# Optimization experiments

Measured on AMD Instinct MI355X. Metric: run time of the kernel, lower is better.

## Reference

```python
import jax, jax.numpy as jnp
import numpy as np

GROUP_SIZE = 64  # quantization group size along in_features (K)


def setup_inputs() -> dict:
    key = jax.random.key(0)
    k1, k2, k3, k4, k5 = jax.random.split(key, 5)
    M, K, N = 32, 8192, 8192
    num_groups = K // GROUP_SIZE
    x = jax.random.normal(k1, (M, K), dtype=jnp.float32)
    # packed int4 weights: two nibbles per byte along K -> [N, K//2]
    packed_weight = jax.random.randint(k2, (N, K // 2), 0, 256, dtype=jnp.int32)
    scales = jax.random.uniform(k3, (N, num_groups), dtype=jnp.float32) * 0.02 + 1e-3
    zeros = jax.random.uniform(k4, (N, num_groups), dtype=jnp.float32) * 15.0
    bias_param = jax.random.normal(k5, (N,), dtype=jnp.float32)
    return {"x": x, "packed_weight": packed_weight, "scales": scales,
            "zeros": zeros, "bias_param": bias_param}


def reference(x, packed_weight, scales, zeros, bias_param):
    # x: [M, K] float; packed_weight: [N, K//2] int (uint8 semantics)
    # scales/zeros: [N, num_groups]; bias_param: [N]
    K = x.shape[-1]
    k = jnp.arange(K)
    shift = (k % 2) * 4                     # low nibble for even k, high for odd
    # unpack int4: q[n, k] in [0, 15]
    q = (packed_weight[:, k // 2] >> shift[None, :]) & 15   # [N, K]
    gidx = k // GROUP_SIZE                                  # [K]
    # group-wise dequant: (q - zero) * scale
    w = (q.astype(jnp.float32) - zeros[:, gidx]) * scales[:, gidx]  # [N, K]
    out = jnp.einsum('mk,nk->mn', x, w) + bias_param[None, :]        # [M, N]
    return out
```

## Files before the change

### kernel.cpp

```cpp
#include <hip/hip_runtime.h>
#include <hip/hip_bf16.h>


#define KK 8192
#define NN 8192
#define KP 4096
#define NG 128
#define BN 16
#define KSW 64
#define NKS 256

typedef __attribute__((ext_vector_type(8))) short short8;
typedef __attribute__((ext_vector_type(4))) float floatx4;

__device__ __forceinline__ unsigned pack_bf16x2(float lo, float hi) {
    union { __hip_bfloat162 h; unsigned u; } c;
    c.h = __float22bfloat162_rn(make_float2(lo, hi));
    return c.u;
}

__global__ void xconv_kernel(const float* __restrict__ x, ushort* __restrict__ xb)
{
    const int tid = blockIdx.x * 256 + threadIdx.x;
    const int l   = tid & 63;
    const int ks  = (tid >> 6) & 255;
    const int mt  = tid >> 14;
    const int m   = (l & 15) + 16 * mt;
    const int kb  = ks * 32 + (l >> 4) * 8;
    const float* src = x + (size_t)m * KK + kb;
    const float4 a = *(const float4*)(src);
    const float4 b = *(const float4*)(src + 4);
    *(uint4*)(xb + (size_t)tid * 8) =
        make_uint4(pack_bf16x2(a.x, a.y), pack_bf16x2(a.z, a.w),
                   pack_bf16x2(b.x, b.y), pack_bf16x2(b.z, b.w));
}

template<bool USE_WS>
__global__ __launch_bounds__(256, 2)
void gptq_mfma_kernel(const int*   __restrict__ pw,
                      const float* __restrict__ scales,
                      const float* __restrict__ zeros,
                      const float* __restrict__ bias,
                      const ushort* __restrict__ xb,
                      const float* __restrict__ x,
                      float* __restrict__ out)
{
    __shared__ float s_lds[NG][BN];
    __shared__ float z_lds[NG][BN];
    __shared__ float red[4][2][256];

    const int tid  = threadIdx.x;
    const int lane = tid & 63;
    const int wave = tid >> 6;
    const int n0   = blockIdx.x * BN;

#pragma unroll
    for (int t = 0; t < 2; ++t) {
        const int e4 = t * 256 + tid;
        const int r  = e4 >> 5;
        const int gb = (e4 & 31) * 4;
        const float4 s4 = *(const float4*)(scales + (size_t)(n0 + r) * NG + gb);
        const float4 z4 = *(const float4*)(zeros  + (size_t)(n0 + r) * NG + gb);
        s_lds[gb + 0][r] = s4.x; s_lds[gb + 1][r] = s4.y;
        s_lds[gb + 2][r] = s4.z; s_lds[gb + 3][r] = s4.w;
        z_lds[gb + 0][r] = z4.x; z_lds[gb + 1][r] = z4.y;
        z_lds[gb + 2][r] = z4.z; z_lds[gb + 3][r] = z4.w;
    }
    __syncthreads();

    const int nl = lane & 15;
    const int kq = lane >> 4;
    const int* pwp = pw + (size_t)(n0 + nl) * KP + kq * 4;
    const uint4* xfp = (const uint4*)xb;
    const int ks0 = wave * KSW;

    const int xm0 = nl;
    const int xkq = kq * 8;

    auto load_xfrag = [&](int mt, int ks) -> uint4 {
        if (USE_WS) {
            return xfp[(size_t)(mt * NKS + ks) * 64 + lane];
        } else {
            const float* src = x + (size_t)(xm0 + 16 * mt) * KK + ks * 32 + xkq;
            const float4 a = *(const float4*)(src);
            const float4 b = *(const float4*)(src + 4);
            return make_uint4(pack_bf16x2(a.x, a.y), pack_bf16x2(a.z, a.w),
                              pack_bf16x2(b.x, b.y), pack_bf16x2(b.z, b.w));
        }
    };

    floatx4 acc0 = {0.f, 0.f, 0.f, 0.f};
    floatx4 acc1 = {0.f, 0.f, 0.f, 0.f};

    int4  pwb[4];
    uint4 x0b[4], x1b[4];

#pragma unroll
    for (int i = 0; i < 3; ++i) {
        const int ks = ks0 + i;
        pwb[i] = *(const int4*)(pwp + ks * 16);
        x0b[i] = load_xfrag(0, ks);
        x1b[i] = load_xfrag(1, ks);
    }

#pragma unroll 4
    for (int i = 0; i < KSW; ++i) {
        const int slot = i & 3;
        if (i + 3 < KSW) {
            const int ks = ks0 + i + 3;
            const int ps = (i + 3) & 3;
            pwb[ps] = *(const int4*)(pwp + ks * 16);
            x0b[ps] = load_xfrag(0, ks);
            x1b[ps] = load_xfrag(1, ks);
        }
        const int ks  = ks0 + i;
        const int g   = ks >> 1;
        const float sc = s_lds[g][nl];
        const float zs = -z_lds[g][nl] * sc;

        union { uint4 v; short8 s; } bf;
        const int4 p = pwb[slot];
        bf.v.x = pack_bf16x2(fmaf((float)(p.x & 15), sc, zs),
                             fmaf((float)((p.x >> 4) & 15), sc, zs));
        bf.v.y = pack_bf16x2(fmaf((float)(p.y & 15), sc, zs),
                             fmaf((float)((p.y >> 4) & 15), sc, zs));
        bf.v.z = pack_bf16x2(fmaf((float)(p.z & 15), sc, zs),
                             fmaf((float)((p.z >> 4) & 15), sc, zs));
        bf.v.w = pack_bf16x2(fmaf((float)(p.w & 15), sc, zs),
                             fmaf((float)((p.w >> 4) & 15), sc, zs));

        union { uint4 v; short8 s; } a0, a1;
        a0.v = x0b[slot];
        a1.v = x1b[slot];
        acc0 = __builtin_amdgcn_mfma_f32_16x16x32_bf16(a0.s, bf.s, acc0, 0, 0, 0);
        acc1 = __builtin_amdgcn_mfma_f32_16x16x32_bf16(a1.s, bf.s, acc1, 0, 0, 0);
    }

#pragma unroll
    for (int r = 0; r < 4; ++r) {
        const int row = kq * 4 + r;
        red[wave][0][row * 16 + nl] = acc0[r];
        red[wave][1][row * 16 + nl] = acc1[r];
    }
    __syncthreads();

#pragma unroll
    for (int i = 0; i < 2; ++i) {
        const int e   = i * 256 + tid;
        const int mt  = e >> 8;
        const int idx = e & 255;
        const float s = red[0][mt][idx] + red[1][mt][idx] + red[2][mt][idx] + red[3][mt][idx];
        const int row = idx >> 4, col = idx & 15;
        const int n   = n0 + col;
        out[(size_t)(mt * 16 + row) * NN + n] = s + bias[n];
    }
}

extern "C" void kernel_launch(void* const* d_in, const int* in_sizes, int n_in,
                              void* d_out, int out_size, void* d_ws, size_t ws_size,
                              hipStream_t stream) {
    const float* x      = (const float*)d_in[0];
    const int*   pw     = (const int*)  d_in[1];
    const float* scales = (const float*)d_in[2];
    const float* zeros  = (const float*)d_in[3];
    const float* bias   = (const float*)d_in[4];
    float* out = (float*)d_out;

    const size_t need = (size_t)32768 * 16;
    if (d_ws != nullptr && ws_size >= need) {
        ushort* xb = (ushort*)d_ws;
        xconv_kernel<<<128, 256, 0, stream>>>(x, xb);
        gptq_mfma_kernel<true><<<512, 256, 0, stream>>>(pw, scales, zeros, bias, xb, x, out);
    } else {
        gptq_mfma_kernel<false><<<512, 256, 0, stream>>>(pw, scales, zeros, bias,
                                                         (const ushort*)nullptr, x, out);
    }
}
```

Baseline: 220.1 us.

## Split K across two blocks with atomic accumulation and bias prefill

```diff
diff --git a/kernel.cpp b/kernel.cpp
--- a/kernel.cpp
+++ b/kernel.cpp
@@ -7,7 +7,8 @@
 #define KP 4096
 #define NG 128
 #define BN 16
-#define KSW 64
+#define KSPLIT 2
+#define KSW 32
 #define NKS 256
 
 typedef __attribute__((ext_vector_type(8))) short short8;
@@ -19,48 +20,57 @@
     return c.u;
 }
 
-__global__ void xconv_kernel(const float* __restrict__ x, ushort* __restrict__ xb)
+__global__ void prep_kernel(const float* __restrict__ x, const float* __restrict__ bias,
+                            ushort* __restrict__ xb, float* __restrict__ out,
+                            int xconv_blocks)
 {
-    const int tid = blockIdx.x * 256 + threadIdx.x;
-    const int l   = tid & 63;
-    const int ks  = (tid >> 6) & 255;
-    const int mt  = tid >> 14;
-    const int m   = (l & 15) + 16 * mt;
-    const int kb  = ks * 32 + (l >> 4) * 8;
-    const float* src = x + (size_t)m * KK + kb;
-    const float4 a = *(const float4*)(src);
-    const float4 b = *(const float4*)(src + 4);
-    *(uint4*)(xb + (size_t)tid * 8) =
-        make_uint4(pack_bf16x2(a.x, a.y), pack_bf16x2(a.z, a.w),
-                   pack_bf16x2(b.x, b.y), pack_bf16x2(b.z, b.w));
+    const int bx = blockIdx.x;
+    if (bx < xconv_blocks) {
+        const int tid = bx * 256 + threadIdx.x;
+        const int l   = tid & 63;
+        const int ks  = (tid >> 6) & 255;
+        const int mt  = tid >> 14;
+        const int m   = (l & 15) + 16 * mt;
+        const int kb  = ks * 32 + (l >> 4) * 8;
+        const float* src = x + (size_t)m * KK + kb;
+        const float4 a = *(const float4*)(src);
+        const float4 b = *(const float4*)(src + 4);
+        *(uint4*)(xb + (size_t)tid * 8) =
+            make_uint4(pack_bf16x2(a.x, a.y), pack_bf16x2(a.z, a.w),
+                       pack_bf16x2(b.x, b.y), pack_bf16x2(b.z, b.w));
+    } else {
+        const int f4 = (bx - xconv_blocks) * 256 + threadIdx.x;
+        const int n4 = f4 & (NN / 4 - 1);
+        const float4 b4 = ((const float4*)bias)[n4];
+        ((float4*)out)[f4] = b4;
+    }
 }
 
 template<bool USE_WS>
-__global__ __launch_bounds__(256, 2)
+__global__ __launch_bounds__(256, 4)
 void gptq_mfma_kernel(const int*   __restrict__ pw,
                       const float* __restrict__ scales,
                       const float* __restrict__ zeros,
-                      const float* __restrict__ bias,
                       const ushort* __restrict__ xb,
                       const float* __restrict__ x,
                       float* __restrict__ out)
 {
-    __shared__ float s_lds[NG][BN];
-    __shared__ float z_lds[NG][BN];
+    __shared__ float s_lds[64][BN + 1];
+    __shared__ float z_lds[64][BN + 1];
     __shared__ float red[4][2][256];
 
     const int tid  = threadIdx.x;
     const int lane = tid & 63;
     const int wave = tid >> 6;
-    const int n0   = blockIdx.x * BN;
+    const int kh   = blockIdx.x & (KSPLIT - 1);
+    const int n0   = (blockIdx.x >> 1) * BN;
+    const int g0   = kh * 64;
 
-#pragma unroll
-    for (int t = 0; t < 2; ++t) {
-        const int e4 = t * 256 + tid;
-        const int r  = e4 >> 5;
-        const int gb = (e4 & 31) * 4;
-        const float4 s4 = *(const float4*)(scales + (size_t)(n0 + r) * NG + gb);
-        const float4 z4 = *(const float4*)(zeros  + (size_t)(n0 + r) * NG + gb);
+    {
+        const int r  = tid >> 4;
+        const int gb = (tid & 15) * 4;
+        const float4 s4 = *(const float4*)(scales + (size_t)(n0 + r) * NG + g0 + gb);
+        const float4 z4 = *(const float4*)(zeros  + (size_t)(n0 + r) * NG + g0 + gb);
         s_lds[gb + 0][r] = s4.x; s_lds[gb + 1][r] = s4.y;
         s_lds[gb + 2][r] = s4.z; s_lds[gb + 3][r] = s4.w;
         z_lds[gb + 0][r] = z4.x; z_lds[gb + 1][r] = z4.y;
@@ -72,7 +82,7 @@
     const int kq = lane >> 4;
     const int* pwp = pw + (size_t)(n0 + nl) * KP + kq * 4;
     const uint4* xfp = (const uint4*)xb;
-    const int ks0 = wave * KSW;
+    const int ks0 = kh * 128 + wave * KSW;
 
     const int xm0 = nl;
     const int xkq = kq * 8;
@@ -113,10 +123,9 @@
             x0b[ps] = load_xfrag(0, ks);
             x1b[ps] = load_xfrag(1, ks);
         }
-        const int ks  = ks0 + i;
-        const int g   = ks >> 1;
-        const float sc = s_lds[g][nl];
-        const float zs = -z_lds[g][nl] * sc;
+        const int gl  = (wave * KSW + i) >> 1;
+        const float sc = s_lds[gl][nl];
+        const float zs = -z_lds[gl][nl] * sc;
 
         union { uint4 v; short8 s; } bf;
         const int4 p = pwb[slot];
@@ -151,8 +160,7 @@
         const int idx = e & 255;
         const float s = red[0][mt][idx] + red[1][mt][idx] + red[2][mt][idx] + red[3][mt][idx];
         const int row = idx >> 4, col = idx & 15;
-        const int n   = n0 + col;
-        out[(size_t)(mt * 16 + row) * NN + n] = s + bias[n];
+        atomicAdd(out + (size_t)(mt * 16 + row) * NN + n0 + col, s);
     }
 }
 
@@ -167,12 +175,15 @@
     float* out = (float*)d_out;
 
     const size_t need = (size_t)32768 * 16;
-    if (d_ws != nullptr && ws_size >= need) {
+    const bool use_ws = (d_ws != nullptr && ws_size >= need);
+
+    if (use_ws) {
         ushort* xb = (ushort*)d_ws;
-        xconv_kernel<<<128, 256, 0, stream>>>(x, xb);
-        gptq_mfma_kernel<true><<<512, 256, 0, stream>>>(pw, scales, zeros, bias, xb, x, out);
+        prep_kernel<<<128 + 256, 256, 0, stream>>>(x, bias, xb, out, 128);
+        gptq_mfma_kernel<true><<<512 * KSPLIT, 256, 0, stream>>>(pw, scales, zeros, xb, x, out);
     } else {
-        gptq_mfma_kernel<false><<<512, 256, 0, stream>>>(pw, scales, zeros, bias,
-                                                         (const ushort*)nullptr, x, out);
+        prep_kernel<<<256, 256, 0, stream>>>(x, bias, nullptr, out, 0);
+        gptq_mfma_kernel<false><<<512 * KSPLIT, 256, 0, stream>>>(pw, scales, zeros,
+                                                                  (const ushort*)nullptr, x, out);
     }
 }
```

Result: faster. 214.6 us (-2.5%).
